# Performance work log

Hardware: AMD Instinct MI355X
Metric: run time of the kernel (lower is better)

The kernel has to match this reference:

```python
import jax, jax.numpy as jnp
import numpy as np


def setup_inputs() -> dict:
    key = jax.random.key(0)
    k1, k2 = jax.random.split(key)
    B, C, H, W = 1, 3, 3500, 2500
    src = jax.random.normal(k1, (B, C, H, W), dtype=jnp.float32)
    flow = jax.random.normal(k2, (B, 2, H, W), dtype=jnp.float32)
    return {"src": src, "flow": flow}


def reference(src, flow):
    """SpatialTransformer.forward: flow + identity grid -> normalize -> bilinear
    grid_sample (zeros padding, align_corners=True). Returns (warped, norm_grid).
    src:  [B, C, H, W] float
    flow: [B, 2, H, W] float; channel 0 = x (width) displacement, channel 1 = y.
    """
    B, C, H, W = src.shape
    dt = flow.dtype
    xs = jnp.arange(W, dtype=dt)  # identity x coords
    ys = jnp.arange(H, dtype=dt)  # identity y coords
    gx = flow[:, 0] + xs[None, None, :]  # [B, H, W] absolute x coord
    gy = flow[:, 1] + ys[None, :, None]  # [B, H, W] absolute y coord
    # normalize to [-1, 1]; max_extent = (W-1, H-1) per torch code
    nx = 2.0 * gx / (W - 1) - 1.0
    ny = 2.0 * gy / (H - 1) - 1.0
    norm_grid = jnp.stack([nx, ny], axis=-1)  # [B, H, W, 2], second output

    # grid_sample with align_corners=True: unnormalize back to pixel coords
    ix = (nx + 1.0) * 0.5 * (W - 1)
    iy = (ny + 1.0) * 0.5 * (H - 1)
    x0 = jnp.floor(ix)
    y0 = jnp.floor(iy)
    x1 = x0 + 1.0
    y1 = y0 + 1.0
    wx1 = ix - x0
    wx0 = 1.0 - wx1
    wy1 = iy - y0
    wy0 = 1.0 - wy1

    def gather(xi, yi):
        # zeros padding: out-of-range corners contribute 0
        valid = (xi >= 0) & (xi <= W - 1) & (yi >= 0) & (yi <= H - 1)
        xc = jnp.clip(xi, 0, W - 1).astype(jnp.int32)
        yc = jnp.clip(yi, 0, H - 1).astype(jnp.int32)
        vals = jax.vmap(lambda sb, yb, xb: sb[:, yb, xb])(src, yc, xc)  # [B,C,H,W]
        return vals * valid.astype(src.dtype)[:, None]

    out = (gather(x0, y0) * (wx0 * wy0)[:, None]
           + gather(x1, y0) * (wx1 * wy0)[:, None]
           + gather(x0, y1) * (wx0 * wy1)[:, None]
           + gather(x1, y1) * (wx1 * wy1)[:, None])
    return out, norm_grid
```

## Files before the change

kernel.cpp:

```cpp
#include <hip/hip_runtime.h>

#define HH 3500
#define WW 2500
#define TXs 64
#define TYs 16
#define WIN_H 24
#define WIN_W 76
#define WIN_W4 19
#define NSTG (3*WIN_H*WIN_W4)
#define NTX 40
#define NTY 219
#define NXCD 8

typedef float f32x4 __attribute__((ext_vector_type(4)));
typedef const __attribute__((address_space(1))) float gfloat;
typedef __attribute__((address_space(3))) float lfloat;

__global__ __launch_bounds__(256, 7) void st_warp_v14(
    const float* __restrict__ src,
    const float* __restrict__ flow,
    float* __restrict__ out)
{
    __shared__ float smf[3 * WIN_H * WIN_W];

    const int nwg = NTX * NTY;
    const int cpx = nwg / NXCD;
    const int bid = blockIdx.x;
    const int sbid = (bid % NXCD) * cpx + bid / NXCD;
    const int xt = sbid / NTY;
    const int yt = sbid - xt * NTY;

    const int tx0 = xt * TXs;
    const int ty0 = yt * TYs;
    const int cx0 = tx0 - 4;
    const int ry0 = ty0 - 4;

    const int wxlo = max(cx0, 0);
    const int wxhi = min(cx0 + WIN_W - 1, WW - 1);
    const int wylo = max(ry0, 0);
    const int wyhi = min(ry0 + WIN_H - 1, HH - 1);

    const long HW = (long)HH * WW;
    const int tid = threadIdx.x;
    const bool colsafe = (cx0 >= 0) && (cx0 + WIN_W <= WW);

    const int r  = tid >> 4;
    const int xb = tx0 + (tid & 15) * 4;
    const int y  = ty0 + r;
    const bool active = (xb < WW) && (y < HH);
    const long idx = (long)y * WW + xb;

    f32x4 fx4 = {0,0,0,0}, fy4 = {0,0,0,0};
    if (active) {
        fx4 = __builtin_nontemporal_load(reinterpret_cast<const f32x4*>(flow + idx));
        fy4 = __builtin_nontemporal_load(reinterpret_cast<const f32x4*>(flow + HW + idx));
    }

    if (colsafe) {
#pragma unroll
        for (int i = 0; i < 6; ++i) {
            const int e = tid + i * 256;
            if (e < NSTG) {
                const int c   = e / (WIN_H * WIN_W4);
                const int rem = e - c * (WIN_H * WIN_W4);
                const int rr  = rem / WIN_W4;
                const int v   = rem - rr * WIN_W4;
                int gy = ry0 + rr; gy = min(max(gy, 0), HH - 1);
                const float* g = src + (long)c * HW + (long)gy * WW + (cx0 + 4 * v);
                __builtin_amdgcn_global_load_lds(
                    (gfloat*)g, (lfloat*)&smf[4 * e], 16, 0, 0);
            }
        }
    } else {
        for (int e = tid; e < 3 * WIN_H * WIN_W; e += 256) {
            const int c   = e / (WIN_H * WIN_W);
            const int rem = e - c * (WIN_H * WIN_W);
            const int rr  = rem / WIN_W;
            const int j   = rem - rr * WIN_W;
            int gy = ry0 + rr; gy = min(max(gy, 0), HH - 1);
            int gx = cx0 + j;  gx = min(max(gx, 0), WW - 1);
            smf[e] = src[(long)c * HW + (long)gy * WW + gx];
        }
    }

    float w00[4], w10[4], w01[4], w11[4];
    float ngv[8];
    int   lb[4];
    int   p0[4];
    int   p1[4];
    int   inwin_mask = 0;

    if (active) {
#pragma unroll
        for (int k = 0; k < 4; ++k) {
            const int x = xb + k;
            const float gx = fx4[k] + (float)x;
            const float gy = fy4[k] + (float)y;

            const float nx = 2.0f * gx / (float)(WW - 1) - 1.0f;
            const float ny = 2.0f * gy / (float)(HH - 1) - 1.0f;
            ngv[2 * k]     = nx;
            ngv[2 * k + 1] = ny;

            const float ixp = (nx + 1.0f) * 0.5f * (float)(WW - 1);
            const float iyp = (ny + 1.0f) * 0.5f * (float)(HH - 1);

            const float x0f = floorf(ixp), y0f = floorf(iyp);
            const float wx1 = ixp - x0f, wx0 = 1.0f - wx1;
            const float wy1 = iyp - y0f, wy0 = 1.0f - wy1;

            const int x0 = (int)x0f, y0i = (int)y0f;
            const int x1 = x0 + 1,  y1i = y0i + 1;

            const bool vx0 = (x0  >= 0) & (x0  < WW);
            const bool vx1 = (x1  >= 0) & (x1  < WW);
            const bool vy0 = (y0i >= 0) & (y0i < HH);
            const bool vy1 = (y1i >= 0) & (y1i < HH);

            w00[k] = wx0 * wy0 * ((vx0 & vy0) ? 1.0f : 0.0f);
            w10[k] = wx1 * wy0 * ((vx1 & vy0) ? 1.0f : 0.0f);
            w01[k] = wx0 * wy1 * ((vx0 & vy1) ? 1.0f : 0.0f);
            w11[k] = wx1 * wy1 * ((vx1 & vy1) ? 1.0f : 0.0f);

            const int x0c = min(max(x0,  0), WW - 1);
            const int y0c = min(max(y0i, 0), HH - 1);
            const int x1c = min(max(x1,  0), WW - 1);
            const int y1c = min(max(y1i, 0), HH - 1);
            p0[k] = (y0c << 16) | x0c;
            p1[k] = (y1c << 16) | x1c;

            const bool inwin = (x0 >= wxlo) & (x1 <= wxhi) &
                               (y0i >= wylo) & (y1i <= wyhi);
            inwin_mask |= (inwin ? 1 : 0) << k;

            lb[k] = (y0i - ry0) * WIN_W + (x0 - cx0);
        }
    }

    __syncthreads();

    if (!active) return;

#pragma unroll
    for (int c = 0; c < 3; ++c) {
        const float* __restrict__ buf = &smf[c * WIN_H * WIN_W];
        float o[4];
#pragma unroll
        for (int k = 0; k < 4; ++k) {
            if ((inwin_mask >> k) & 1) {
                const float* b = buf + lb[k];
                o[k] = b[0] * w00[k] + b[1] * w10[k]
                     + b[WIN_W] * w01[k] + b[WIN_W + 1] * w11[k];
            } else {
                const int x0c = p0[k] & 0xffff, y0c = p0[k] >> 16;
                const int x1c = p1[k] & 0xffff, y1c = p1[k] >> 16;
                const float* __restrict__ s = src + (long)c * HW;
                o[k] = s[(long)y0c * WW + x0c] * w00[k]
                     + s[(long)y0c * WW + x1c] * w10[k]
                     + s[(long)y1c * WW + x0c] * w01[k]
                     + s[(long)y1c * WW + x1c] * w11[k];
            }
        }
        f32x4 v = {o[0], o[1], o[2], o[3]};
        __builtin_nontemporal_store(v, reinterpret_cast<f32x4*>(out + (long)c * HW + idx));
    }
    float* ngbase = out + 3 * HW + 2 * idx;
    f32x4 n0 = {ngv[0], ngv[1], ngv[2], ngv[3]};
    f32x4 n1 = {ngv[4], ngv[5], ngv[6], ngv[7]};
    __builtin_nontemporal_store(n0, reinterpret_cast<f32x4*>(ngbase));
    __builtin_nontemporal_store(n1, reinterpret_cast<f32x4*>(ngbase + 4));
}

extern "C" void kernel_launch(void* const* d_in, const int* in_sizes, int n_in,
                              void* d_out, int out_size, void* d_ws, size_t ws_size,
                              hipStream_t stream) {
    const float* src  = (const float*)d_in[0];
    const float* flow = (const float*)d_in[1];
    float* out = (float*)d_out;
    (void)d_ws; (void)ws_size; (void)in_sizes; (void)n_in; (void)out_size;

    dim3 block(256, 1, 1);
    dim3 grid(NTX * NTY, 1, 1);
    st_warp_v14<<<grid, block, 0, stream>>>(src, flow, out);
}
```

Baseline: 103.0 us.

## Stage per-wave source windows in LDS and replace block barrier with waitcnt

```diff
diff --git a/kernel.cpp b/kernel.cpp
--- a/kernel.cpp
+++ b/kernel.cpp
@@ -4,10 +4,12 @@
 #define WW 2500
 #define TXs 64
 #define TYs 16
-#define WIN_H 24
+#define WIN_H 13
 #define WIN_W 76
 #define WIN_W4 19
-#define NSTG (3*WIN_H*WIN_W4)
+#define CPLANE (WIN_H*WIN_W4)
+#define NSTG_W (3*CPLANE)
+#define WWORDS (3*WIN_H*WIN_W)
 #define NTX 40
 #define NTY 219
 #define NXCD 8
@@ -16,12 +18,12 @@
 typedef const __attribute__((address_space(1))) float gfloat;
 typedef __attribute__((address_space(3))) float lfloat;
 
-__global__ __launch_bounds__(256, 7) void st_warp_v14(
+__global__ __launch_bounds__(256, 3) void st_warp_v15(
     const float* __restrict__ src,
     const float* __restrict__ flow,
     float* __restrict__ out)
 {
-    __shared__ float smf[3 * WIN_H * WIN_W];
+    __shared__ float smw[4 * WWORDS];
 
     const int nwg = NTX * NTY;
     const int cpx = nwg / NXCD;
@@ -33,20 +35,25 @@
     const int tx0 = xt * TXs;
     const int ty0 = yt * TYs;
     const int cx0 = tx0 - 4;
-    const int ry0 = ty0 - 4;
 
+    const long HW = (long)HH * WW;
+    const int tid  = threadIdx.x;
+    const int wave = tid >> 6;
+    const int lane = tid & 63;
+    const bool colsafe = (cx0 >= 0) && (cx0 + WIN_W <= WW);
+
+    const int wy0  = ty0 + wave * 4;
+    const int ry0w = wy0 - 4;
     const int wxlo = max(cx0, 0);
     const int wxhi = min(cx0 + WIN_W - 1, WW - 1);
-    const int wylo = max(ry0, 0);
-    const int wyhi = min(ry0 + WIN_H - 1, HH - 1);
+    const int wylo = max(ry0w, 0);
+    const int wyhi = min(ry0w + WIN_H - 1, HH - 1);
 
-    const long HW = (long)HH * WW;
-    const int tid = threadIdx.x;
-    const bool colsafe = (cx0 >= 0) && (cx0 + WIN_W <= WW);
+    float* const wseg = smw + wave * WWORDS;
 
-    const int r  = tid >> 4;
-    const int xb = tx0 + (tid & 15) * 4;
-    const int y  = ty0 + r;
+    const int r  = lane >> 4;
+    const int xb = tx0 + (lane & 15) * 4;
+    const int y  = wy0 + r;
     const bool active = (xb < WW) && (y < HH);
     const long idx = (long)y * WW + xb;
 
@@ -58,36 +65,36 @@
 
     if (colsafe) {
 #pragma unroll
-        for (int i = 0; i < 6; ++i) {
-            const int e = tid + i * 256;
-            if (e < NSTG) {
-                const int c   = e / (WIN_H * WIN_W4);
-                const int rem = e - c * (WIN_H * WIN_W4);
+        for (int i = 0; i < 12; ++i) {
+            const int e = lane + i * 64;
+            if (e < NSTG_W) {
+                const int c   = e / CPLANE;
+                const int rem = e - c * CPLANE;
                 const int rr  = rem / WIN_W4;
                 const int v   = rem - rr * WIN_W4;
-                int gy = ry0 + rr; gy = min(max(gy, 0), HH - 1);
+                int gy = ry0w + rr; gy = min(max(gy, 0), HH - 1);
                 const float* g = src + (long)c * HW + (long)gy * WW + (cx0 + 4 * v);
                 __builtin_amdgcn_global_load_lds(
-                    (gfloat*)g, (lfloat*)&smf[4 * e], 16, 0, 0);
+                    (gfloat*)g, (lfloat*)&wseg[4 * e], 16, 0, 0);
             }
         }
     } else {
-        for (int e = tid; e < 3 * WIN_H * WIN_W; e += 256) {
+        for (int e = lane; e < 3 * WIN_H * WIN_W; e += 64) {
             const int c   = e / (WIN_H * WIN_W);
             const int rem = e - c * (WIN_H * WIN_W);
             const int rr  = rem / WIN_W;
             const int j   = rem - rr * WIN_W;
-            int gy = ry0 + rr; gy = min(max(gy, 0), HH - 1);
-            int gx = cx0 + j;  gx = min(max(gx, 0), WW - 1);
-            smf[e] = src[(long)c * HW + (long)gy * WW + gx];
+            int gy = ry0w + rr; gy = min(max(gy, 0), HH - 1);
+            int gx = cx0 + j;   gx = min(max(gx, 0), WW - 1);
+            wseg[c * (WIN_H * WIN_W) + rr * WIN_W + j] =
+                src[(long)c * HW + (long)gy * WW + gx];
         }
     }
 
     float w00[4], w10[4], w01[4], w11[4];
     float ngv[8];
     int   lb[4];
-    int   p0[4];
-    int   p1[4];
+    int   p0[4], p1[4];
     int   inwin_mask = 0;
 
     if (active) {
@@ -133,17 +140,17 @@
                                (y0i >= wylo) & (y1i <= wyhi);
             inwin_mask |= (inwin ? 1 : 0) << k;
 
-            lb[k] = (y0i - ry0) * WIN_W + (x0 - cx0);
+            lb[k] = (y0i - ry0w) * WIN_W + (x0 - cx0);
         }
     }
 
-    __syncthreads();
+    asm volatile("s_waitcnt vmcnt(0) lgkmcnt(0)" ::: "memory");
 
     if (!active) return;
 
 #pragma unroll
     for (int c = 0; c < 3; ++c) {
-        const float* __restrict__ buf = &smf[c * WIN_H * WIN_W];
+        const float* __restrict__ buf = wseg + c * (WIN_H * WIN_W);
         float o[4];
 #pragma unroll
         for (int k = 0; k < 4; ++k) {
@@ -181,5 +188,5 @@
 
     dim3 block(256, 1, 1);
     dim3 grid(NTX * NTY, 1, 1);
-    st_warp_v14<<<grid, block, 0, stream>>>(src, flow, out);
+    st_warp_v15<<<grid, block, 0, stream>>>(src, flow, out);
 }
```

Result: slower. 112.9 us (+9.6%).
